# Kernel optimization log

Hardware: AMD Instinct MI355X
Metric: run time of the kernel (lower is better)

## Reference

```python
import jax, jax.numpy as jnp
import numpy as np

N_NODES = 100000
N_EDGES = 1600000
IN_DIM = 128
HEADS = 4
OUT_DIM = 32
NEG_SLOPE = 0.2  # PyG GATConv default negative_slope


def setup_inputs() -> dict:
    key = jax.random.key(0)
    k_x, k_e, k_w, k_as, k_ad = jax.random.split(key, 5)
    x = jax.random.normal(k_x, (N_NODES, IN_DIM), dtype=jnp.float32)
    edge_index = jax.random.randint(k_e, (2, N_EDGES), 0, N_NODES, dtype=jnp.int64)
    # Glorot-style init for learned parameters (GATConv lin + attention vectors)
    W = jax.random.normal(k_w, (IN_DIM, HEADS * OUT_DIM), dtype=jnp.float32) / np.sqrt(IN_DIM)
    att_src = jax.random.normal(k_as, (HEADS, OUT_DIM), dtype=jnp.float32) / np.sqrt(OUT_DIM)
    att_dst = jax.random.normal(k_ad, (HEADS, OUT_DIM), dtype=jnp.float32) / np.sqrt(OUT_DIM)
    bias = jnp.zeros((HEADS * OUT_DIM,), dtype=jnp.float32)
    return {"x": x, "edge_index": edge_index, "W": W, "att_src": att_src,
            "att_dst": att_dst, "bias": bias}


def reference(x, edge_index, W, att_src, att_dst, bias):
    N = x.shape[0]
    H, D = att_src.shape
    # PyG GATConv default: add self loops
    loop = jnp.arange(N, dtype=edge_index.dtype)
    src = jnp.concatenate([edge_index[0], loop])  # message sources  [E+N]
    dst = jnp.concatenate([edge_index[1], loop])  # message targets  [E+N]

    h = (x @ W).reshape(N, H, D)                          # [N, H, D]
    a_src = jnp.einsum('nhd,hd->nh', h, att_src)          # [N, H]
    a_dst = jnp.einsum('nhd,hd->nh', h, att_dst)          # [N, H]

    # per-edge attention logits, LeakyReLU(neg_slope=0.2)
    e = jax.nn.leaky_relu(a_src[src] + a_dst[dst], NEG_SLOPE)  # [E+N, H]

    # segment softmax over edges grouped by target node (numerically stable)
    e_max = jax.ops.segment_max(e, dst, num_segments=N)        # [N, H]
    e_max = jnp.where(jnp.isfinite(e_max), e_max, jnp.float32(0))
    ex = jnp.exp(e - e_max[dst])                               # [E+N, H]
    denom = jax.ops.segment_sum(ex, dst, num_segments=N)       # [N, H]
    alpha = ex / (denom[dst] + jnp.float32(1e-16))             # [E+N, H]

    # weighted scatter-aggregate of source features
    msg = h[src] * alpha[:, :, None]                           # [E+N, H, D]
    out = jax.ops.segment_sum(msg, dst, num_segments=N)        # [N, H, D]
    out = out.reshape(N, H * D) + bias                         # concat heads + bias
    return jax.nn.elu(out)                                     # wrapper ELU
```

## Files before the change

### kernel.cpp

```cpp
#include <hip/hip_runtime.h>
#include <hip/hip_fp16.h>
#include <math.h>

#define N_NODES 100000
#define N_EDGES 1600000
#define IN_DIM 128
#define F_DIM 128
#define NEG_SLOPE 0.2f

#define BUCKW_LOG 7
#define NBUCK 784
#define NBLK 128
#define EPB 12500
#define G_TOT (NBUCK * NBLK)
#define SC_CHUNK 4096
#define SC_NB ((G_TOT + SC_CHUNK - 1) / SC_CHUNK)
#define CSR_CAP (N_EDGES + NBUCK * 384)

typedef short v8s __attribute__((ext_vector_type(8)));
typedef float v4f __attribute__((ext_vector_type(4)));

static __device__ __forceinline__ unsigned short f2bf(float f) {
    unsigned u = __float_as_uint(f);
    u += 0x7fffu + ((u >> 16) & 1u);
    return (unsigned short)(u >> 16);
}
static __device__ __forceinline__ float bf2f(unsigned s) { return __uint_as_float(s << 16); }
static __device__ __forceinline__ float lo2f(unsigned u) { return __uint_as_float(u << 16); }
static __device__ __forceinline__ float hi2f(unsigned u) { return __uint_as_float(u & 0xffff0000u); }

__global__ __launch_bounds__(256) void k_wprep(const float* __restrict__ W,
                                               unsigned short* __restrict__ Wt) {
    int i = blockIdx.x * 256 + threadIdx.x;
    int n = i >> 7, k = i & 127;
    Wt[n * 128 + k] = f2bf(W[k * 128 + n]);
}

__global__ __launch_bounds__(256) void k_gemm(const float* __restrict__ x,
                                              const unsigned short* __restrict__ Wt,
                                              unsigned short* __restrict__ h16,
                                              const float* __restrict__ att_src,
                                              const float* __restrict__ att_dst,
                                              float* __restrict__ a_src,
                                              float* __restrict__ a_dst) {
    __shared__ unsigned short As[64][136];
    __shared__ unsigned short Bs[128][136];
    __shared__ float attl[256];
    const int t  = threadIdx.x;
    const int n0 = blockIdx.x * 64;

    attl[t] = (t < 128) ? att_src[t] : att_dst[t - 128];

    {
        int row = t >> 2, k0 = (t & 3) * 32;
        int n = n0 + row;
        #pragma unroll
        for (int i = 0; i < 4; i++) {
            float4 va = make_float4(0.f,0.f,0.f,0.f), vb = va;
            if (n < N_NODES) {
                const float* p = x + (size_t)n * IN_DIM + k0 + i * 8;
                va = *(const float4*)p;
                vb = *(const float4*)(p + 4);
            }
            uint4 u;
            u.x = f2bf(va.x) | ((unsigned)f2bf(va.y) << 16);
            u.y = f2bf(va.z) | ((unsigned)f2bf(va.w) << 16);
            u.z = f2bf(vb.x) | ((unsigned)f2bf(vb.y) << 16);
            u.w = f2bf(vb.z) | ((unsigned)f2bf(vb.w) << 16);
            *(uint4*)&As[row][k0 + i * 8] = u;
        }
    }
    {
        int nr = t >> 1, s0 = (t & 1) * 64;
        const uint4* src = (const uint4*)(Wt + nr * 128 + s0);
        #pragma unroll
        for (int i = 0; i < 8; i++)
            *(uint4*)&Bs[nr][s0 + i * 8] = src[i];
    }
    __syncthreads();

    const int w = t >> 6, lane = t & 63;
    const int mr = lane & 15, quad = lane >> 4;
    const int m0 = w * 16;

    v4f acc[8];
    #pragma unroll
    for (int nt = 0; nt < 8; nt++) acc[nt] = (v4f){0.f, 0.f, 0.f, 0.f};

    #pragma unroll
    for (int kk = 0; kk < 4; kk++) {
        int kof = kk * 32 + quad * 8;
        v8s a = *(const v8s*)&As[m0 + mr][kof];
        #pragma unroll
        for (int nt = 0; nt < 8; nt++) {
            v8s b = *(const v8s*)&Bs[nt * 16 + mr][kof];
            acc[nt] = __builtin_amdgcn_mfma_f32_16x16x32_bf16(a, b, acc[nt], 0, 0, 0);
        }
    }

    #pragma unroll
    for (int nt = 0; nt < 8; nt++)
        #pragma unroll
        for (int r = 0; r < 4; r++)
            As[m0 + quad * 4 + r][nt * 16 + mr] = f2bf(acc[nt][r]);
    __syncthreads();
    {
        int row = m0 + (lane >> 2);
        int c0  = (lane & 3) * 32;
        int n = n0 + row;
        if (n < N_NODES) {
            float ds = 0.f, dd = 0.f;
            #pragma unroll
            for (int i = 0; i < 4; i++) {
                uint4 v = *(const uint4*)&As[row][c0 + i * 8];
                *(uint4*)&h16[(size_t)n * F_DIM + c0 + i * 8] = v;
                float f0 = lo2f(v.x), f1 = hi2f(v.x);
                float f2 = lo2f(v.y), f3 = hi2f(v.y);
                float f4 = lo2f(v.z), f5 = hi2f(v.z);
                float f6 = lo2f(v.w), f7 = hi2f(v.w);
                const float* ps = &attl[c0 + i * 8];
                const float* pd = &attl[128 + c0 + i * 8];
                ds += f0*ps[0] + f1*ps[1] + f2*ps[2] + f3*ps[3]
                    + f4*ps[4] + f5*ps[5] + f6*ps[6] + f7*ps[7];
                dd += f0*pd[0] + f1*pd[1] + f2*pd[2] + f3*pd[3]
                    + f4*pd[4] + f5*pd[5] + f6*pd[6] + f7*pd[7];
            }
            int hd = lane & 3;
            a_src[n * 4 + hd] = ds;
            a_dst[n * 4 + hd] = dd;
        }
    }
}

__global__ __launch_bounds__(256) void k_bhist(const int* __restrict__ ei_dst,
                                               int* __restrict__ G) {
    __shared__ int hist[NBUCK];
    for (int i = threadIdx.x; i < NBUCK; i += 256) hist[i] = 0;
    __syncthreads();
    int e0 = blockIdx.x * EPB;
    for (int i = threadIdx.x; i < EPB; i += 256) {
        int d = ei_dst[e0 + i];
        atomicAdd(&hist[d >> BUCKW_LOG], 1);
    }
    __syncthreads();
    for (int b = threadIdx.x; b < NBUCK; b += 256)
        G[b * NBLK + blockIdx.x] = hist[b];
}

__global__ __launch_bounds__(256) void k_scanp(const int* __restrict__ a,
                                               int* __restrict__ part) {
    int base = blockIdx.x * SC_CHUNK + threadIdx.x * 16;
    int s = 0;
    #pragma unroll
    for (int i = 0; i < 16; i++) {
        int idx = base + i;
        if (idx < G_TOT) s += a[idx];
    }
    __shared__ int wsum[4];
    for (int off = 32; off >= 1; off >>= 1) s += __shfl_down(s, off, 64);
    if ((threadIdx.x & 63) == 0) wsum[threadIdx.x >> 6] = s;
    __syncthreads();
    if (threadIdx.x == 0) part[blockIdx.x] = wsum[0] + wsum[1] + wsum[2] + wsum[3];
}

__global__ void k_scant(int* part, int* boff) {
    int lane = threadIdx.x & 63;
    int v = (lane < SC_NB) ? part[lane] : 0;
    int x = v;
    #pragma unroll
    for (int off = 1; off < 64; off <<= 1) {
        int y = __shfl_up(x, off, 64);
        if (lane >= off) x += y;
    }
    if (lane < SC_NB) part[lane] = x - v;
    if (lane == 0) boff[NBUCK] = N_EDGES;
}

__global__ __launch_bounds__(256) void k_scand(int* __restrict__ a,
                                               const int* __restrict__ part,
                                               int* __restrict__ boff) {
    __shared__ int tsum[256];
    int tid  = threadIdx.x;
    int base = blockIdx.x * SC_CHUNK + tid * 16;
    int v[16]; int s = 0;
    #pragma unroll
    for (int i = 0; i < 16; i++) {
        int idx = base + i;
        v[i] = (idx < G_TOT) ? a[idx] : 0;
        s += v[i];
    }
    tsum[tid] = s;
    __syncthreads();
    for (int off = 1; off < 256; off <<= 1) {
        int y = (tid >= off) ? tsum[tid - off] : 0;
        __syncthreads();
        tsum[tid] += y;
        __syncthreads();
    }
    int run = part[blockIdx.x] + tsum[tid] - s;
    #pragma unroll
    for (int i = 0; i < 16; i++) {
        int idx = base + i;
        if (idx < G_TOT) {
            a[idx] = run;
            if (idx % NBLK == 0) boff[idx / NBLK] = run;
        }
        run += v[i];
    }
}

__global__ __launch_bounds__(256) void k_bscat(const int* __restrict__ ei,
                                               const int* __restrict__ G,
                                               int* __restrict__ ebuf) {
    __shared__ int base[NBUCK];
    for (int b = threadIdx.x; b < NBUCK; b += 256)
        base[b] = G[b * NBLK + blockIdx.x];
    __syncthreads();
    int e0 = blockIdx.x * EPB;
    for (int i = threadIdx.x; i < EPB; i += 256) {
        int s = ei[e0 + i];
        int d = ei[N_EDGES + e0 + i];
        int b = d >> BUCKW_LOG;
        int pos = atomicAdd(&base[b], 1);
        ebuf[pos] = s | ((d & 127) << 17);
    }
}

__global__ __launch_bounds__(256) void k_csrfin(const int* __restrict__ ebuf,
                                                const int* __restrict__ boff,
                                                const float* __restrict__ a_src,
                                                const float* __restrict__ a_dst,
                                                int2* __restrict__ ebounds,
                                                int* __restrict__ csr2,
                                                __half* __restrict__ pbuf) {
    __shared__ int cnt[128];
    __shared__ int off[128];
    int b = blockIdx.x;
    int beg = boff[b], end = boff[b + 1];
    int padded_base = beg + b * 384;
    if (threadIdx.x < 128) cnt[threadIdx.x] = 0;
    __syncthreads();
    for (int j = beg + threadIdx.x; j < end; j += 256)
        atomicAdd(&cnt[(ebuf[j] >> 17) & 127], 1);
    __syncthreads();
    if (threadIdx.x == 0) {
        int run = padded_base;
        for (int i = 0; i < 128; i++) { off[i] = run; run += (cnt[i] + 3) & ~3; }
    }
    __syncthreads();
    if (threadIdx.x < 128) {
        int node = (b << BUCKW_LOG) + threadIdx.x;
        int c = cnt[threadIdx.x];
        if (node < N_NODES) {
            ebounds[node] = make_int2(off[threadIdx.x], off[threadIdx.x] + c);
            int cpad = (c + 3) & ~3;
            for (int k = c; k < cpad; k++) {
                int pos = off[threadIdx.x] + k;
                csr2[pos] = node;
                *(uint2*)&pbuf[(size_t)pos * 4] = make_uint2(0u, 0u);
            }
        }
        cnt[threadIdx.x] = 0;
    }
    __syncthreads();
    for (int j = beg + threadIdx.x; j < end; j += 256) {
        int p = ebuf[j];
        int dl = (p >> 17) & 127;
        int s = p & 0x1ffff;
        int r = atomicAdd(&cnt[dl], 1);
        int pos = off[dl] + r;
        csr2[pos] = s;
        int d = (b << BUCKW_LOG) + dl;
        float4 as = *(const float4*)&a_src[s * 4];
        float4 ad = *(const float4*)&a_dst[d * 4];
        float e0 = as.x + ad.x; e0 = e0 > 0.f ? e0 : NEG_SLOPE * e0;
        float e1 = as.y + ad.y; e1 = e1 > 0.f ? e1 : NEG_SLOPE * e1;
        float e2 = as.z + ad.z; e2 = e2 > 0.f ? e2 : NEG_SLOPE * e2;
        float e3 = as.w + ad.w; e3 = e3 > 0.f ? e3 : NEG_SLOPE * e3;
        __half2 lo = __floats2half2_rn(__expf(e0), __expf(e1));
        __half2 hi = __floats2half2_rn(__expf(e2), __expf(e3));
        *(uint2*)&pbuf[(size_t)pos * 4] =
            make_uint2(*(unsigned*)&lo, *(unsigned*)&hi);
    }
}

__global__ __launch_bounds__(256) void k_agg(const uint4* __restrict__ h16x4,
                                             const float* __restrict__ a_src,
                                             const float* __restrict__ a_dst,
                                             const int2* __restrict__ ebounds,
                                             const int* __restrict__ csr2,
                                             const __half* __restrict__ pbuf,
                                             const float* __restrict__ bias,
                                             float* __restrict__ out) {
    int n = (blockIdx.x * 256 + threadIdx.x) >> 6;
    if (n >= N_NODES) return;
    int lane = threadIdx.x & 63;
    int grp = lane >> 4, g = lane & 15, hd = g >> 2;

    float p0 = 0.f;
    if (grp == 0) {
        float e0 = a_src[n * 4 + hd] + a_dst[n * 4 + hd];
        e0 = e0 > 0.f ? e0 : NEG_SLOPE * e0;
        p0 = __expf(e0);
    }
    uint4 hs = h16x4[(size_t)n * 16 + g];
    float l  = p0;
    float a0 = p0 * lo2f(hs.x), a1 = p0 * hi2f(hs.x);
    float a2 = p0 * lo2f(hs.y), a3 = p0 * hi2f(hs.y);
    float a4 = p0 * lo2f(hs.z), a5 = p0 * hi2f(hs.z);
    float a6 = p0 * lo2f(hs.w), a7 = p0 * hi2f(hs.w);

    int2 eb = ebounds[n];
    int beg = eb.x, cnt = eb.y - eb.x;
    const int* sp = csr2 + beg + grp;
    const __half* pp = pbuf + (size_t)(beg + grp) * 4 + hd;
    int steps = (cnt + 3) >> 2;
    int t = 0;
    for (; t + 2 <= steps; t += 2) {
        int s0 = sp[4 * t];
        int s1 = sp[4 * t + 4];
        float q0 = __half2float(pp[16 * t]);
        float q1 = __half2float(pp[16 * t + 16]);
        uint4 h0 = h16x4[(size_t)s0 * 16 + g];
        uint4 h1 = h16x4[(size_t)s1 * 16 + g];
        l  += q0 + q1;
        a0 += q0 * lo2f(h0.x) + q1 * lo2f(h1.x);
        a1 += q0 * hi2f(h0.x) + q1 * hi2f(h1.x);
        a2 += q0 * lo2f(h0.y) + q1 * lo2f(h1.y);
        a3 += q0 * hi2f(h0.y) + q1 * hi2f(h1.y);
        a4 += q0 * lo2f(h0.z) + q1 * lo2f(h1.z);
        a5 += q0 * hi2f(h0.z) + q1 * hi2f(h1.z);
        a6 += q0 * lo2f(h0.w) + q1 * lo2f(h1.w);
        a7 += q0 * hi2f(h0.w) + q1 * hi2f(h1.w);
    }
    if (t < steps) {
        int s0 = sp[4 * t];
        float q0 = __half2float(pp[16 * t]);
        uint4 h0 = h16x4[(size_t)s0 * 16 + g];
        l  += q0;
        a0 += q0 * lo2f(h0.x);
        a1 += q0 * hi2f(h0.x);
        a2 += q0 * lo2f(h0.y);
        a3 += q0 * hi2f(h0.y);
        a4 += q0 * lo2f(h0.z);
        a5 += q0 * hi2f(h0.z);
        a6 += q0 * lo2f(h0.w);
        a7 += q0 * hi2f(h0.w);
    }
    #define RED2(v) v += __shfl_xor(v, 16, 64); v += __shfl_xor(v, 32, 64);
    RED2(l); RED2(a0); RED2(a1); RED2(a2); RED2(a3);
    RED2(a4); RED2(a5); RED2(a6); RED2(a7);
    #undef RED2

    if (grp == 0) {
        float inv = 1.f / (l + 1e-16f);
        float4 b0 = *(const float4*)&bias[g * 8];
        float4 b1 = *(const float4*)&bias[g * 8 + 4];
        float o0 = a0 * inv + b0.x, o1 = a1 * inv + b0.y;
        float o2 = a2 * inv + b0.z, o3 = a3 * inv + b0.w;
        float o4 = a4 * inv + b1.x, o5 = a5 * inv + b1.y;
        float o6 = a6 * inv + b1.z, o7 = a7 * inv + b1.w;
        o0 = o0 > 0.f ? o0 : __expf(o0) - 1.f;
        o1 = o1 > 0.f ? o1 : __expf(o1) - 1.f;
        o2 = o2 > 0.f ? o2 : __expf(o2) - 1.f;
        o3 = o3 > 0.f ? o3 : __expf(o3) - 1.f;
        o4 = o4 > 0.f ? o4 : __expf(o4) - 1.f;
        o5 = o5 > 0.f ? o5 : __expf(o5) - 1.f;
        o6 = o6 > 0.f ? o6 : __expf(o6) - 1.f;
        o7 = o7 > 0.f ? o7 : __expf(o7) - 1.f;
        *(float4*)&out[(size_t)n * F_DIM + g * 8]     = make_float4(o0, o1, o2, o3);
        *(float4*)&out[(size_t)n * F_DIM + g * 8 + 4] = make_float4(o4, o5, o6, o7);
    }
}

extern "C" void kernel_launch(void* const* d_in, const int* in_sizes, int n_in,
                              void* d_out, int out_size, void* d_ws, size_t ws_size,
                              hipStream_t stream) {
    const float* x       = (const float*)d_in[0];
    const int*   ei      = (const int*)d_in[1];
    const float* W       = (const float*)d_in[2];
    const float* att_src = (const float*)d_in[3];
    const float* att_dst = (const float*)d_in[4];
    const float* bias    = (const float*)d_in[5];
    float*       out     = (float*)d_out;

    char* ws = (char*)d_ws;
    unsigned short* h16 = (unsigned short*)ws; ws += (size_t)N_NODES * F_DIM * 2;
    unsigned short* Wt  = (unsigned short*)ws; ws += (size_t)IN_DIM * F_DIM * 2;
    float* a_src  = (float*)ws; ws += (size_t)N_NODES * 4 * 4;
    float* a_dst  = (float*)ws; ws += (size_t)N_NODES * 4 * 4;
    int*   G      = (int*)ws;   ws += (size_t)G_TOT * 4;
    int*   part   = (int*)ws;   ws += 1024;
    int*   boff   = (int*)ws;   ws += 4096;
    int2*  ebounds= (int2*)ws;  ws += (size_t)N_NODES * 8 + 512;
    int*   ebuf   = (int*)ws;   ws += (size_t)N_EDGES * 4;
    int*   csr2   = (int*)ws;   ws += (size_t)CSR_CAP * 4;
    __half* pbuf  = (__half*)ws; ws += (size_t)CSR_CAP * 4 * 2;

    k_wprep<<<64, 256, 0, stream>>>(W, Wt);
    k_gemm<<<(N_NODES + 63) / 64, 256, 0, stream>>>(x, Wt, h16, att_src, att_dst, a_src, a_dst);

    k_bhist<<<NBLK, 256, 0, stream>>>(ei + N_EDGES, G);
    k_scanp<<<SC_NB, 256, 0, stream>>>(G, part);
    k_scant<<<1, 64, 0, stream>>>(part, boff);
    k_scand<<<SC_NB, 256, 0, stream>>>(G, part, boff);
    k_bscat<<<NBLK, 256, 0, stream>>>(ei, G, ebuf);
    k_csrfin<<<NBUCK, 256, 0, stream>>>(ebuf, boff, a_src, a_dst, ebounds, csr2, pbuf);

    k_agg<<<(N_NODES * 64 + 255) / 256, 256, 0, stream>>>((const uint4*)h16, a_src, a_dst, ebounds, csr2, pbuf, bias, out);
}
```

Before: 301.0 us.

## Widen CSR build kernels, vectorize edge loads, warp-scan offsets, unroll aggregation by four

The histogram and bucket-scatter kernels move from 256 to 1024 threads per block and read edge indices as int4, so the 128 blocks get more memory parallelism. The CSR finalize kernel uses 512 threads, unrolls its loops by four, and replaces the serial single-thread offset prefix with a wavefront shuffle scan. The aggregation loop is unrolled from two to four neighbor gathers per step to keep more loads in flight. Risks are higher register pressure in the aggregation kernel and more LDS atomic contention with larger blocks. The int4 loads also rely on each block's edge range being 16-byte aligned, which holds because EPB=12500 is a multiple of four.

After: 268.7 us. 1.12x faster.

```diff
diff --git a/kernel.cpp b/kernel.cpp
--- a/kernel.cpp
+++ b/kernel.cpp
@@ -132,18 +132,22 @@
     }
 }
 
-__global__ __launch_bounds__(256) void k_bhist(const int* __restrict__ ei_dst,
-                                               int* __restrict__ G) {
+__global__ __launch_bounds__(1024) void k_bhist(const int* __restrict__ ei_dst,
+                                                int* __restrict__ G) {
     __shared__ int hist[NBUCK];
-    for (int i = threadIdx.x; i < NBUCK; i += 256) hist[i] = 0;
-    __syncthreads();
-    int e0 = blockIdx.x * EPB;
-    for (int i = threadIdx.x; i < EPB; i += 256) {
-        int d = ei_dst[e0 + i];
-        atomicAdd(&hist[d >> BUCKW_LOG], 1);
-    }
-    __syncthreads();
-    for (int b = threadIdx.x; b < NBUCK; b += 256)
+    for (int i = threadIdx.x; i < NBUCK; i += 1024) hist[i] = 0;
+    __syncthreads();
+    const int4* p = (const int4*)(ei_dst + blockIdx.x * EPB);
+    const int n4 = EPB / 4;
+    for (int i = threadIdx.x; i < n4; i += 1024) {
+        int4 d = p[i];
+        atomicAdd(&hist[d.x >> BUCKW_LOG], 1);
+        atomicAdd(&hist[d.y >> BUCKW_LOG], 1);
+        atomicAdd(&hist[d.z >> BUCKW_LOG], 1);
+        atomicAdd(&hist[d.w >> BUCKW_LOG], 1);
+    }
+    __syncthreads();
+    for (int b = threadIdx.x; b < NBUCK; b += 1024)
         G[b * NBLK + blockIdx.x] = hist[b];
 }
 
@@ -209,24 +213,31 @@
     }
 }
 
-__global__ __launch_bounds__(256) void k_bscat(const int* __restrict__ ei,
-                                               const int* __restrict__ G,
-                                               int* __restrict__ ebuf) {
+__global__ __launch_bounds__(1024) void k_bscat(const int* __restrict__ ei,
+                                                const int* __restrict__ G,
+                                                int* __restrict__ ebuf) {
     __shared__ int base[NBUCK];
-    for (int b = threadIdx.x; b < NBUCK; b += 256)
+    for (int b = threadIdx.x; b < NBUCK; b += 1024)
         base[b] = G[b * NBLK + blockIdx.x];
     __syncthreads();
-    int e0 = blockIdx.x * EPB;
-    for (int i = threadIdx.x; i < EPB; i += 256) {
-        int s = ei[e0 + i];
-        int d = ei[N_EDGES + e0 + i];
-        int b = d >> BUCKW_LOG;
-        int pos = atomicAdd(&base[b], 1);
-        ebuf[pos] = s | ((d & 127) << 17);
-    }
-}
-
-__global__ __launch_bounds__(256) void k_csrfin(const int* __restrict__ ebuf,
+    const int4* ps = (const int4*)(ei + blockIdx.x * EPB);
+    const int4* pd = (const int4*)(ei + N_EDGES + blockIdx.x * EPB);
+    const int n4 = EPB / 4;
+    for (int i = threadIdx.x; i < n4; i += 1024) {
+        int4 s = ps[i];
+        int4 d = pd[i];
+        int b0 = d.x >> BUCKW_LOG; int p0 = atomicAdd(&base[b0], 1);
+        ebuf[p0] = s.x | ((d.x & 127) << 17);
+        int b1 = d.y >> BUCKW_LOG; int p1 = atomicAdd(&base[b1], 1);
+        ebuf[p1] = s.y | ((d.y & 127) << 17);
+        int b2 = d.z >> BUCKW_LOG; int p2 = atomicAdd(&base[b2], 1);
+        ebuf[p2] = s.z | ((d.z & 127) << 17);
+        int b3 = d.w >> BUCKW_LOG; int p3 = atomicAdd(&base[b3], 1);
+        ebuf[p3] = s.w | ((d.w & 127) << 17);
+    }
+}
+
+__global__ __launch_bounds__(512) void k_csrfin(const int* __restrict__ ebuf,
                                                 const int* __restrict__ boff,
                                                 const float* __restrict__ a_src,
                                                 const float* __restrict__ a_dst,
@@ -235,53 +246,91 @@
                                                 __half* __restrict__ pbuf) {
     __shared__ int cnt[128];
     __shared__ int off[128];
+    __shared__ int wtot;
     int b = blockIdx.x;
     int beg = boff[b], end = boff[b + 1];
     int padded_base = beg + b * 384;
-    if (threadIdx.x < 128) cnt[threadIdx.x] = 0;
-    __syncthreads();
-    for (int j = beg + threadIdx.x; j < end; j += 256)
-        atomicAdd(&cnt[(ebuf[j] >> 17) & 127], 1);
-    __syncthreads();
-    if (threadIdx.x == 0) {
-        int run = padded_base;
-        for (int i = 0; i < 128; i++) { off[i] = run; run += (cnt[i] + 3) & ~3; }
-    }
-    __syncthreads();
-    if (threadIdx.x < 128) {
-        int node = (b << BUCKW_LOG) + threadIdx.x;
-        int c = cnt[threadIdx.x];
+    int tid = threadIdx.x;
+    if (tid < 128) cnt[tid] = 0;
+    __syncthreads();
+    {
+        int j = beg + tid;
+        for (; j + 3 * 512 < end; j += 4 * 512) {
+            int e0 = ebuf[j];
+            int e1 = ebuf[j + 512];
+            int e2 = ebuf[j + 1024];
+            int e3 = ebuf[j + 1536];
+            atomicAdd(&cnt[(e0 >> 17) & 127], 1);
+            atomicAdd(&cnt[(e1 >> 17) & 127], 1);
+            atomicAdd(&cnt[(e2 >> 17) & 127], 1);
+            atomicAdd(&cnt[(e3 >> 17) & 127], 1);
+        }
+        for (; j < end; j += 512)
+            atomicAdd(&cnt[(ebuf[j] >> 17) & 127], 1);
+    }
+    __syncthreads();
+    if (tid < 128) {
+        int cp = (cnt[tid] + 3) & ~3;
+        int x = cp;
+        #pragma unroll
+        for (int o = 1; o < 64; o <<= 1) {
+            int y = __shfl_up(x, o, 64);
+            if ((tid & 63) >= o) x += y;
+        }
+        off[tid] = x - cp;
+        if (tid == 63) wtot = x;
+    }
+    __syncthreads();
+    if (tid < 128) {
+        int v = off[tid] + ((tid >= 64) ? wtot : 0) + padded_base;
+        off[tid] = v;
+        int node = (b << BUCKW_LOG) + tid;
+        int c = cnt[tid];
         if (node < N_NODES) {
-            ebounds[node] = make_int2(off[threadIdx.x], off[threadIdx.x] + c);
+            ebounds[node] = make_int2(v, v + c);
             int cpad = (c + 3) & ~3;
             for (int k = c; k < cpad; k++) {
-                int pos = off[threadIdx.x] + k;
+                int pos = v + k;
                 csr2[pos] = node;
                 *(uint2*)&pbuf[(size_t)pos * 4] = make_uint2(0u, 0u);
             }
         }
-        cnt[threadIdx.x] = 0;
-    }
-    __syncthreads();
-    for (int j = beg + threadIdx.x; j < end; j += 256) {
-        int p = ebuf[j];
-        int dl = (p >> 17) & 127;
-        int s = p & 0x1ffff;
-        int r = atomicAdd(&cnt[dl], 1);
-        int pos = off[dl] + r;
-        csr2[pos] = s;
-        int d = (b << BUCKW_LOG) + dl;
-        float4 as = *(const float4*)&a_src[s * 4];
-        float4 ad = *(const float4*)&a_dst[d * 4];
-        float e0 = as.x + ad.x; e0 = e0 > 0.f ? e0 : NEG_SLOPE * e0;
-        float e1 = as.y + ad.y; e1 = e1 > 0.f ? e1 : NEG_SLOPE * e1;
-        float e2 = as.z + ad.z; e2 = e2 > 0.f ? e2 : NEG_SLOPE * e2;
-        float e3 = as.w + ad.w; e3 = e3 > 0.f ? e3 : NEG_SLOPE * e3;
-        __half2 lo = __floats2half2_rn(__expf(e0), __expf(e1));
-        __half2 hi = __floats2half2_rn(__expf(e2), __expf(e3));
-        *(uint2*)&pbuf[(size_t)pos * 4] =
-            make_uint2(*(unsigned*)&lo, *(unsigned*)&hi);
-    }
+        cnt[tid] = 0;
+    }
+    __syncthreads();
+    #define PLACE(pv) {                                                        \
+        int dl = ((pv) >> 17) & 127;                                           \
+        int s  = (pv) & 0x1ffff;                                               \
+        int r = atomicAdd(&cnt[dl], 1);                                        \
+        int pos = off[dl] + r;                                                 \
+        csr2[pos] = s;                                                         \
+        int d = (b << BUCKW_LOG) + dl;                                         \
+        float4 as = *(const float4*)&a_src[s * 4];                             \
+        float4 ad = *(const float4*)&a_dst[d * 4];                             \
+        float e0 = as.x + ad.x; e0 = e0 > 0.f ? e0 : NEG_SLOPE * e0;           \
+        float e1 = as.y + ad.y; e1 = e1 > 0.f ? e1 : NEG_SLOPE * e1;           \
+        float e2 = as.z + ad.z; e2 = e2 > 0.f ? e2 : NEG_SLOPE * e2;           \
+        float e3 = as.w + ad.w; e3 = e3 > 0.f ? e3 : NEG_SLOPE * e3;           \
+        __half2 lo = __floats2half2_rn(__expf(e0), __expf(e1));                \
+        __half2 hi = __floats2half2_rn(__expf(e2), __expf(e3));                \
+        *(uint2*)&pbuf[(size_t)pos * 4] =                                      \
+            make_uint2(*(unsigned*)&lo, *(unsigned*)&hi);                      \
+    }
+    {
+        int j = beg + tid;
+        for (; j + 3 * 512 < end; j += 4 * 512) {
+            int e0 = ebuf[j];
+            int e1 = ebuf[j + 512];
+            int e2 = ebuf[j + 1024];
+            int e3 = ebuf[j + 1536];
+            PLACE(e0); PLACE(e1); PLACE(e2); PLACE(e3);
+        }
+        for (; j < end; j += 512) {
+            int e0 = ebuf[j];
+            PLACE(e0);
+        }
+    }
+    #undef PLACE
 }
 
 __global__ __launch_bounds__(256) void k_agg(const uint4* __restrict__ h16x4,
@@ -316,24 +365,30 @@
     const __half* pp = pbuf + (size_t)(beg + grp) * 4 + hd;
     int steps = (cnt + 3) >> 2;
     int t = 0;
-    for (; t + 2 <= steps; t += 2) {
+    for (; t + 4 <= steps; t += 4) {
         int s0 = sp[4 * t];
         int s1 = sp[4 * t + 4];
+        int s2 = sp[4 * t + 8];
+        int s3 = sp[4 * t + 12];
         float q0 = __half2float(pp[16 * t]);
         float q1 = __half2float(pp[16 * t + 16]);
+        float q2 = __half2float(pp[16 * t + 32]);
+        float q3 = __half2float(pp[16 * t + 48]);
         uint4 h0 = h16x4[(size_t)s0 * 16 + g];
         uint4 h1 = h16x4[(size_t)s1 * 16 + g];
-        l  += q0 + q1;
-        a0 += q0 * lo2f(h0.x) + q1 * lo2f(h1.x);
-        a1 += q0 * hi2f(h0.x) + q1 * hi2f(h1.x);
-        a2 += q0 * lo2f(h0.y) + q1 * lo2f(h1.y);
-        a3 += q0 * hi2f(h0.y) + q1 * hi2f(h1.y);
-        a4 += q0 * lo2f(h0.z) + q1 * lo2f(h1.z);
-        a5 += q0 * hi2f(h0.z) + q1 * hi2f(h1.z);
-        a6 += q0 * lo2f(h0.w) + q1 * lo2f(h1.w);
-        a7 += q0 * hi2f(h0.w) + q1 * hi2f(h1.w);
-    }
-    if (t < steps) {
+        uint4 h2 = h16x4[(size_t)s2 * 16 + g];
+        uint4 h3 = h16x4[(size_t)s3 * 16 + g];
+        l  += (q0 + q1) + (q2 + q3);
+        a0 += q0 * lo2f(h0.x) + q1 * lo2f(h1.x) + q2 * lo2f(h2.x) + q3 * lo2f(h3.x);
+        a1 += q0 * hi2f(h0.x) + q1 * hi2f(h1.x) + q2 * hi2f(h2.x) + q3 * hi2f(h3.x);
+        a2 += q0 * lo2f(h0.y) + q1 * lo2f(h1.y) + q2 * lo2f(h2.y) + q3 * lo2f(h3.y);
+        a3 += q0 * hi2f(h0.y) + q1 * hi2f(h1.y) + q2 * hi2f(h2.y) + q3 * hi2f(h3.y);
+        a4 += q0 * lo2f(h0.z) + q1 * lo2f(h1.z) + q2 * lo2f(h2.z) + q3 * lo2f(h3.z);
+        a5 += q0 * hi2f(h0.z) + q1 * hi2f(h1.z) + q2 * hi2f(h2.z) + q3 * hi2f(h3.z);
+        a6 += q0 * lo2f(h0.w) + q1 * lo2f(h1.w) + q2 * lo2f(h2.w) + q3 * lo2f(h3.w);
+        a7 += q0 * hi2f(h0.w) + q1 * hi2f(h1.w) + q2 * hi2f(h2.w) + q3 * hi2f(h3.w);
+    }
+    for (; t < steps; ++t) {
         int s0 = sp[4 * t];
         float q0 = __half2float(pp[16 * t]);
         uint4 h0 = h16x4[(size_t)s0 * 16 + g];
@@ -400,12 +455,12 @@
     k_wprep<<<64, 256, 0, stream>>>(W, Wt);
     k_gemm<<<(N_NODES + 63) / 64, 256, 0, stream>>>(x, Wt, h16, att_src, att_dst, a_src, a_dst);
 
-    k_bhist<<<NBLK, 256, 0, stream>>>(ei + N_EDGES, G);
+    k_bhist<<<NBLK, 1024, 0, stream>>>(ei + N_EDGES, G);
     k_scanp<<<SC_NB, 256, 0, stream>>>(G, part);
     k_scant<<<1, 64, 0, stream>>>(part, boff);
     k_scand<<<SC_NB, 256, 0, stream>>>(G, part, boff);
-    k_bscat<<<NBLK, 256, 0, stream>>>(ei, G, ebuf);
-    k_csrfin<<<NBUCK, 256, 0, stream>>>(ebuf, boff, a_src, a_dst, ebounds, csr2, pbuf);
+    k_bscat<<<NBLK, 1024, 0, stream>>>(ei, G, ebuf);
+    k_csrfin<<<NBUCK, 512, 0, stream>>>(ebuf, boff, a_src, a_dst, ebounds, csr2, pbuf);
 
     k_agg<<<(N_NODES * 64 + 255) / 256, 256, 0, stream>>>((const uint4*)h16, a_src, a_dst, ebounds, csr2, pbuf, bias, out);
 }
```
